# Kernel tuning notes

Hardware: AMD Instinct MI355X
Metric: run time of the kernel (lower is better)

Reference implementation:

```python
import jax, jax.numpy as jnp
import numpy as np

RESERVOIR_SIZE = 1024
D_MODEL = 512
BATCH = 256
SEQ_LEN = 512
SPECTRAL_RADIUS = 0.9
SPARSITY = 0.9
INPUT_SCALING = 1.0


def _build_reservoir_weights(seed=0):
    rng = np.random.default_rng(seed)
    W_in = rng.standard_normal((RESERVOIR_SIZE, 1)).astype(np.float32) * INPUT_SCALING
    W_res = rng.standard_normal((RESERVOIR_SIZE, RESERVOIR_SIZE)).astype(np.float32)
    # sparsify: zero out `sparsity` fraction of entries
    num_zeros = int(RESERVOIR_SIZE * RESERVOIR_SIZE * SPARSITY)
    flat = W_res.reshape(-1)
    zero_idx = rng.permutation(RESERVOIR_SIZE * RESERVOIR_SIZE)[:num_zeros]
    flat[zero_idx] = 0.0
    # rescale to target spectral radius
    eigs = np.linalg.eigvals(W_res.astype(np.float64))
    sr = np.max(np.abs(eigs))
    if sr > 1e-9:
        W_res *= np.float32(SPECTRAL_RADIUS / sr)
    return jnp.asarray(W_in), jnp.asarray(W_res)


def setup_inputs() -> dict:
    key = jax.random.key(0)
    kx, kw, kb = jax.random.split(key, 3)
    x = jax.random.normal(kx, (BATCH, SEQ_LEN), dtype=jnp.float32)
    W_in, W_res = _build_reservoir_weights(0)
    # trainable readout: Linear(reservoir_size, d_model)
    bound = 1.0 / np.sqrt(RESERVOIR_SIZE)
    readout_w = jax.random.uniform(kw, (D_MODEL, RESERVOIR_SIZE), jnp.float32, -bound, bound)
    readout_b = jax.random.uniform(kb, (D_MODEL,), jnp.float32, -bound, bound)
    return {"x": x, "W_in": W_in, "W_res": W_res,
            "readout_w": readout_w, "readout_b": readout_b}


def reference(x, W_in, W_res, readout_w, readout_b):
    # x: [B, S]; recurrence h_{t} = tanh(h_{t-1} @ W_res.T + u_t @ W_in.T)
    B = x.shape[0]
    h0 = jnp.zeros((B, RESERVOIR_SIZE), dtype=x.dtype)
    w_in_row = W_in[:, 0]  # [R]; u_t @ W_in.T == outer(u_t, w_in_row)

    def step(h, u_t):
        # u_t: [B]
        h_new = jnp.tanh(h @ W_res.T + u_t[:, None] * w_in_row[None, :])
        return h_new, None

    h_final, _ = jax.lax.scan(step, h0, x.T)  # scan over seq dim
    return h_final @ readout_w.T + readout_b  # [B, d_model]
```

## Files before the change

kernel.cpp:

```cpp
#include <hip/hip_runtime.h>

#define RES 1024
#define SEQ 512

typedef _Float16 f16;
typedef _Float16 half8 __attribute__((ext_vector_type(8)));
typedef float f32x4 __attribute__((ext_vector_type(4)));
typedef float f32x2 __attribute__((ext_vector_type(2), aligned(4)));
typedef unsigned int uint4v __attribute__((ext_vector_type(4)));

#define PST 35
#define PIDX(w8, n, rr, cc) ((((w8) * 4 + (n)) * 16 + (rr)) * PST + (cc))


__device__ __forceinline__ float fast_tanh(float v) {
  float vc = fminf(15.0f, fmaxf(-15.0f, v));
  float e = __expf(2.0f * vc);
  return (e - 1.0f) * __builtin_amdgcn_rcpf(e + 1.0f);
}

#define FULL_LOAD(ptr)                                                  \
  asm volatile(                                                         \
      "global_load_dwordx4 %0, %4, off sc0 sc1\n\t"                     \
      "global_load_dwordx4 %1, %4, off offset:64 sc0 sc1\n\t"           \
      "global_load_dwordx4 %2, %4, off offset:128 sc0 sc1\n\t"          \
      "global_load_dwordx4 %3, %4, off offset:192 sc0 sc1\n\t"          \
      "s_waitcnt vmcnt(0)"                                              \
      : "=&v"(A0), "=&v"(A1), "=&v"(A2), "=&v"(A3) : "v"(ptr) : "memory")

__device__ __forceinline__ bool tags_ok(half8 A0, half8 A1, half8 A2, half8 A3,
                                        unsigned int tagr) {
  const uint4v b0 = __builtin_bit_cast(uint4v, A0);
  const uint4v b1 = __builtin_bit_cast(uint4v, A1);
  const uint4v b2 = __builtin_bit_cast(uint4v, A2);
  const uint4v b3 = __builtin_bit_cast(uint4v, A3);
  unsigned int d =
      (b0.x ^ tagr) | (b0.y ^ tagr) | (b0.z ^ tagr) | (b0.w ^ tagr) |
      (b1.x ^ tagr) | (b1.y ^ tagr) | (b1.z ^ tagr) | (b1.w ^ tagr) |
      (b2.x ^ tagr) | (b2.y ^ tagr) | (b2.z ^ tagr) | (b2.w ^ tagr) |
      (b3.x ^ tagr) | (b3.y ^ tagr) | (b3.z ^ tagr) | (b3.w ^ tagr);
  return ((d & 1u) == 0u);
}

__global__ __launch_bounds__(512, 2) void res_recur_kernel(
    const float* __restrict__ x,
    const float* __restrict__ W_in,
    const float* __restrict__ W_res,
    f16* __restrict__ hp0,
    f16* __restrict__ hp1,
    f16* __restrict__ hm0,
    f16* __restrict__ hm1,
    unsigned int* __restrict__ xcdmap)
{
  __shared__ float P[20608];
  __shared__ unsigned char xmap_s[256];
  __shared__ int l2mode_s;

  const int tid  = threadIdx.x;
  const int wave = tid >> 6;
  const int lane = tid & 63;
  const int col  = lane & 15;
  const int kq   = (lane >> 4) & 3;

  const int bx = blockIdx.x;
  const int g  = (bx & 7) * 2 + ((bx >> 3) & 1);
  const int w  = bx >> 4;

  unsigned int myxcc;
  asm volatile("s_getreg_b32 %0, hwreg(HW_REG_XCC_ID, 0, 8)" : "=s"(myxcc));
  if (tid == 0)
    __hip_atomic_store(&xcdmap[bx], (myxcc & 0xffu) + 1u, __ATOMIC_RELAXED,
                       __HIP_MEMORY_SCOPE_AGENT);

  half8 Wf[4][4];
#pragma unroll
  for (int n = 0; n < 4; ++n) {
    const float* Wr = W_res + (size_t)(w * 64 + n * 16 + col) * RES + wave * 128 + kq * 8;
#pragma unroll
    for (int ks = 0; ks < 4; ++ks) {
      f32x4 lo = *(const f32x4*)(Wr + ks * 32);
      f32x4 hi = *(const f32x4*)(Wr + ks * 32 + 4);
      half8 f;
#pragma unroll
      for (int j = 0; j < 4; ++j) { f[j] = (f16)lo[j]; f[j + 4] = (f16)hi[j]; }
      Wf[n][ks] = f;
    }
  }

  if (tid < 256) {
    const unsigned int* ap = xcdmap + tid;
    unsigned int v;
    do {
      asm volatile("global_load_dword %0, %1, off sc0 sc1\n\t"
                   "s_waitcnt vmcnt(0)"
                   : "=&v"(v) : "v"(ap) : "memory");
    } while (v == 0u);
    xmap_s[tid] = (unsigned char)v;
  }
  __syncthreads();
  if (tid == 0) {
    const int base = (g >> 1) + 8 * (g & 1);
    const unsigned char ref = xmap_s[base];
    int ok = 1, cnt = 0;
    for (int i = 0; i < 256; ++i) cnt += (xmap_s[i] == ref) ? 1 : 0;
    for (int k = 0; k < 16; ++k) ok &= (xmap_s[base + 16 * k] == ref) ? 1 : 0;
    l2mode_s = (ok && cnt <= 64) ? 1 : 0;
  }
  __syncthreads();
  const bool l2mode = (l2mode_s != 0);

  const int r   = tid >> 5;
  const int cp  = tid & 31;
  const int n_e = cp >> 3;
  const int c0  = (cp & 7) * 2;
  const int rd_off = 12 - 4 * (r >> 2);
  const float win_lo = W_in[w * 64 + n_e * 16 + c0];
  const float win_hi = W_in[w * 64 + n_e * 16 + c0 + 1];
  const float* xr = x + (size_t)(g * 16 + r) * SEQ;
  const unsigned int houtidx = ((unsigned)(g * 16 + r) * RES + w * 64 + n_e * 16 + c0) >> 1;

  const size_t aoff = (size_t)(g * 16 + col) * RES + wave * 128 + kq * 8;

  for (int s = 0; s < SEQ; ++s) {
    float u = xr[s];

    f32x4 acc[4];
#pragma unroll
    for (int n = 0; n < 4; ++n) acc[n] = (f32x4){0.f, 0.f, 0.f, 0.f};

    if (s > 0) {
      const unsigned int tagr = (unsigned)(((s >> 1) + (s & 1)) & 1);
      const f16* Ap = ((s & 1) ? hp1 : hp0) + aoff;
      const f16* Am = ((s & 1) ? hm1 : hm0) + aoff;
      half8 A0, A1, A2, A3;

      FULL_LOAD(Ap);
      bool ok = tags_ok(A0, A1, A2, A3, tagr);
      unsigned int it = 0;
      while (!ok) {
        ++it;
        asm volatile("s_sleep 2");
        const f16* Pp = (!l2mode && ((it & 7u) == 0u)) ? Am : Ap;
        FULL_LOAD(Pp);
        ok = tags_ok(A0, A1, A2, A3, tagr);
      }

#pragma unroll
      for (int n = 0; n < 4; ++n) acc[n] = __builtin_amdgcn_mfma_f32_16x16x32_f16(A0, Wf[n][0], acc[n], 0, 0, 0);
#pragma unroll
      for (int n = 0; n < 4; ++n) acc[n] = __builtin_amdgcn_mfma_f32_16x16x32_f16(A1, Wf[n][1], acc[n], 0, 0, 0);
#pragma unroll
      for (int n = 0; n < 4; ++n) acc[n] = __builtin_amdgcn_mfma_f32_16x16x32_f16(A2, Wf[n][2], acc[n], 0, 0, 0);
#pragma unroll
      for (int n = 0; n < 4; ++n) acc[n] = __builtin_amdgcn_mfma_f32_16x16x32_f16(A3, Wf[n][3], acc[n], 0, 0, 0);
    }

#pragma unroll
    for (int n = 0; n < 4; ++n)
#pragma unroll
      for (int j = 0; j < 4; ++j)
        P[PIDX(wave, n, kq * 4 + j, col) + 12 - 4 * kq] = acc[n][j];

    __syncthreads();

    float s_lo = 0.f, s_hi = 0.f;
#pragma unroll
    for (int w8 = 0; w8 < 8; ++w8) {
      f32x2 t = *(const f32x2*)&P[PIDX(w8, n_e, r, c0) + rd_off];
      s_lo += t.x;
      s_hi += t.y;
    }
    float v_lo = fast_tanh(s_lo + u * win_lo);
    float v_hi = fast_tanh(s_hi + u * win_hi);

    const unsigned int tagw = (unsigned)((((s + 1) >> 1) + ((s + 1) & 1)) & 1);
    union { f16 h[2]; unsigned int u32; } pk;
    pk.h[0] = (f16)v_lo;
    pk.h[1] = (f16)v_hi;
    pk.u32  = (pk.u32 & ~1u) | tagw;

    unsigned int* Hp = (unsigned int*)((s & 1) ? hp0 : hp1);
    Hp[houtidx] = pk.u32;
    if (!l2mode) {
      unsigned int* Hm = (unsigned int*)((s & 1) ? hm0 : hm1);
      __hip_atomic_store(&Hm[houtidx], pk.u32, __ATOMIC_RELAXED,
                         __HIP_MEMORY_SCOPE_AGENT);
    }

    asm volatile("" ::: "memory");
    __builtin_amdgcn_s_barrier();
  }
}

__global__ __launch_bounds__(256) void res_readout_kernel(
    const f16* __restrict__ Hf,
    const float* __restrict__ Wout,
    const float* __restrict__ bout,
    float* __restrict__ out)
{
  __shared__ f16 hs[16][1032];
  __shared__ f16 wsh[32][1032];
  const int tid = threadIdx.x;
  const int bb = blockIdx.x >> 4;
  const int db = blockIdx.x & 15;

  for (int idx = tid; idx < 2048; idx += 256) {
    int row = idx >> 7, cin = idx & 127;
    *(half8*)&hs[row][cin * 8] = *(const half8*)(Hf + (size_t)(bb * 16 + row) * RES + cin * 8);
  }
  for (int idx = tid; idx < 4096; idx += 256) {
    int row = idx >> 7, cin = idx & 127;
    const float* p = Wout + (size_t)(db * 32 + row) * RES + cin * 8;
    f32x4 lo = *(const f32x4*)(p);
    f32x4 hi = *(const f32x4*)(p + 4);
    half8 f;
#pragma unroll
    for (int j = 0; j < 4; ++j) { f[j] = (f16)lo[j]; f[j + 4] = (f16)hi[j]; }
    *(half8*)&wsh[row][cin * 8] = f;
  }
  __syncthreads();

  const int d  = tid & 31;
  const int bp = tid >> 5;
  float acc0 = 0.f, acc1 = 0.f;
  for (int kc = 0; kc < 128; ++kc) {
    half8 wv = *(const half8*)&wsh[d][kc * 8];
    half8 h0 = *(const half8*)&hs[bp * 2][kc * 8];
    half8 h1 = *(const half8*)&hs[bp * 2 + 1][kc * 8];
#pragma unroll
    for (int j = 0; j < 8; ++j) {
      float wf = (float)wv[j];
      acc0 += wf * (float)h0[j];
      acc1 += wf * (float)h1[j];
    }
  }
  float bo = bout[db * 32 + d];
  out[(size_t)(bb * 16 + bp * 2) * 512 + db * 32 + d]     = acc0 + bo;
  out[(size_t)(bb * 16 + bp * 2 + 1) * 512 + db * 32 + d] = acc1 + bo;
}

extern "C" void kernel_launch(void* const* d_in, const int* in_sizes, int n_in,
                              void* d_out, int out_size, void* d_ws, size_t ws_size,
                              hipStream_t stream) {
  (void)in_sizes; (void)n_in; (void)out_size; (void)ws_size;
  const float* x     = (const float*)d_in[0];
  const float* W_in  = (const float*)d_in[1];
  const float* W_res = (const float*)d_in[2];
  const float* Wout  = (const float*)d_in[3];
  const float* bout  = (const float*)d_in[4];
  float* out = (float*)d_out;

  char* ws = (char*)d_ws;
  f16* hp0 = (f16*)(ws);
  f16* hp1 = (f16*)(ws + (512u << 10));
  f16* hm0 = (f16*)(ws + (1024u << 10));
  f16* hm1 = (f16*)(ws + (1536u << 10));
  unsigned int* xcdmap = (unsigned int*)(ws + (2048u << 10));

  hipMemsetAsync(ws, 0, (2048u << 10), stream);
  hipMemsetAsync(ws + (2048u << 10), 0, 1024, stream);

  res_recur_kernel<<<dim3(256), dim3(512), 0, stream>>>(x, W_in, W_res,
                                                        hp0, hp1, hm0, hm1, xcdmap);
  res_readout_kernel<<<dim3(256), dim3(256), 0, stream>>>(hp0, Wout, bout, out);
}
```

Baseline: 866.1 us.

## Split each recurrence step into two 8-row phases and stage x in LDS

```diff
diff --git a/kernel.cpp b/kernel.cpp
--- a/kernel.cpp
+++ b/kernel.cpp
@@ -52,7 +52,8 @@
     f16* __restrict__ hm1,
     unsigned int* __restrict__ xcdmap)
 {
-  __shared__ float P[20608];
+  __shared__ float P[17920];
+  __shared__ float x_s[16][512];
   __shared__ unsigned char xmap_s[256];
   __shared__ int l2mode_s;
 
@@ -63,7 +64,7 @@
   const int kq   = (lane >> 4) & 3;
 
   const int bx = blockIdx.x;
-  const int g  = (bx & 7) * 2 + ((bx >> 3) & 1);
+  const int p  = (bx & 7) * 2 + ((bx >> 3) & 1);
   const int w  = bx >> 4;
 
   unsigned int myxcc;
@@ -85,6 +86,11 @@
       for (int j = 0; j < 4; ++j) { f[j] = (f16)lo[j]; f[j + 4] = (f16)hi[j]; }
       Wf[n][ks] = f;
     }
+  }
+
+  for (int idx = tid; idx < 2048; idx += 512) {
+    int row = idx >> 7, c4 = (idx & 127) * 4;
+    *(f32x4*)&x_s[row][c4] = *(const f32x4*)(x + (size_t)(p * 16 + row) * SEQ + c4);
   }
 
   if (tid < 256) {
@@ -99,7 +105,7 @@
   }
   __syncthreads();
   if (tid == 0) {
-    const int base = (g >> 1) + 8 * (g & 1);
+    const int base = (p >> 1) + 8 * (p & 1);
     const unsigned char ref = xmap_s[base];
     int ok = 1, cnt = 0;
     for (int i = 0; i < 256; ++i) cnt += (xmap_s[i] == ref) ? 1 : 0;
@@ -110,85 +116,91 @@
   const bool l2mode = (l2mode_s != 0);
 
   const int r   = tid >> 5;
+  const int rr  = r & 7;
+  const bool active = (r < 8);
   const int cp  = tid & 31;
   const int n_e = cp >> 3;
   const int c0  = (cp & 7) * 2;
   const int rd_off = 12 - 4 * (r >> 2);
   const float win_lo = W_in[w * 64 + n_e * 16 + c0];
   const float win_hi = W_in[w * 64 + n_e * 16 + c0 + 1];
-  const float* xr = x + (size_t)(g * 16 + r) * SEQ;
-  const unsigned int houtidx = ((unsigned)(g * 16 + r) * RES + w * 64 + n_e * 16 + c0) >> 1;
-
-  const size_t aoff = (size_t)(g * 16 + col) * RES + wave * 128 + kq * 8;
+
+  const size_t aoff0 = (size_t)(p * 16 + (col & 7)) * RES + wave * 128 + kq * 8;
 
   for (int s = 0; s < SEQ; ++s) {
-    float u = xr[s];
-
-    f32x4 acc[4];
-#pragma unroll
-    for (int n = 0; n < 4; ++n) acc[n] = (f32x4){0.f, 0.f, 0.f, 0.f};
-
-    if (s > 0) {
-      const unsigned int tagr = (unsigned)(((s >> 1) + (s & 1)) & 1);
-      const f16* Ap = ((s & 1) ? hp1 : hp0) + aoff;
-      const f16* Am = ((s & 1) ? hm1 : hm0) + aoff;
-      half8 A0, A1, A2, A3;
-
-      FULL_LOAD(Ap);
-      bool ok = tags_ok(A0, A1, A2, A3, tagr);
-      unsigned int it = 0;
-      while (!ok) {
-        ++it;
-        asm volatile("s_sleep 2");
-        const f16* Pp = (!l2mode && ((it & 7u) == 0u)) ? Am : Ap;
-        FULL_LOAD(Pp);
-        ok = tags_ok(A0, A1, A2, A3, tagr);
+    const unsigned int tagr = (unsigned)(((s >> 1) + (s & 1)) & 1);
+    const unsigned int tagw = (unsigned)((((s + 1) >> 1) + ((s + 1) & 1)) & 1);
+
+    for (int ph = 0; ph < 2; ++ph) {
+      const int rb = ph << 3;
+      float u = x_s[rb + rr][s];
+
+      f32x4 acc[4];
+#pragma unroll
+      for (int n = 0; n < 4; ++n) acc[n] = (f32x4){0.f, 0.f, 0.f, 0.f};
+
+      if (s > 0) {
+        const f16* Ap = ((s & 1) ? hp1 : hp0) + aoff0 + (size_t)rb * RES;
+        const f16* Am = ((s & 1) ? hm1 : hm0) + aoff0 + (size_t)rb * RES;
+        half8 A0, A1, A2, A3;
+
+        FULL_LOAD(Ap);
+        bool ok = tags_ok(A0, A1, A2, A3, tagr);
+        unsigned int it = 0;
+        while (!ok) {
+          ++it;
+          const f16* Pp = (!l2mode && ((it & 7u) == 0u)) ? Am : Ap;
+          FULL_LOAD(Pp);
+          ok = tags_ok(A0, A1, A2, A3, tagr);
+        }
+
+#pragma unroll
+        for (int n = 0; n < 4; ++n) acc[n] = __builtin_amdgcn_mfma_f32_16x16x32_f16(A0, Wf[n][0], acc[n], 0, 0, 0);
+#pragma unroll
+        for (int n = 0; n < 4; ++n) acc[n] = __builtin_amdgcn_mfma_f32_16x16x32_f16(A1, Wf[n][1], acc[n], 0, 0, 0);
+#pragma unroll
+        for (int n = 0; n < 4; ++n) acc[n] = __builtin_amdgcn_mfma_f32_16x16x32_f16(A2, Wf[n][2], acc[n], 0, 0, 0);
+#pragma unroll
+        for (int n = 0; n < 4; ++n) acc[n] = __builtin_amdgcn_mfma_f32_16x16x32_f16(A3, Wf[n][3], acc[n], 0, 0, 0);
       }
 
 #pragma unroll
-      for (int n = 0; n < 4; ++n) acc[n] = __builtin_amdgcn_mfma_f32_16x16x32_f16(A0, Wf[n][0], acc[n], 0, 0, 0);
-#pragma unroll
-      for (int n = 0; n < 4; ++n) acc[n] = __builtin_amdgcn_mfma_f32_16x16x32_f16(A1, Wf[n][1], acc[n], 0, 0, 0);
-#pragma unroll
-      for (int n = 0; n < 4; ++n) acc[n] = __builtin_amdgcn_mfma_f32_16x16x32_f16(A2, Wf[n][2], acc[n], 0, 0, 0);
-#pragma unroll
-      for (int n = 0; n < 4; ++n) acc[n] = __builtin_amdgcn_mfma_f32_16x16x32_f16(A3, Wf[n][3], acc[n], 0, 0, 0);
+      for (int n = 0; n < 4; ++n)
+#pragma unroll
+        for (int j = 0; j < 4; ++j)
+          P[PIDX(wave, n, kq * 4 + j, col) + 12 - 4 * kq] = acc[n][j];
+
+      __syncthreads();
+
+      float s_lo = 0.f, s_hi = 0.f;
+#pragma unroll
+      for (int w8 = 0; w8 < 8; ++w8) {
+        f32x2 t = *(const f32x2*)&P[PIDX(w8, n_e, r, c0) + rd_off];
+        s_lo += t.x;
+        s_hi += t.y;
+      }
+      float v_lo = fast_tanh(s_lo + u * win_lo);
+      float v_hi = fast_tanh(s_hi + u * win_hi);
+
+      union { f16 h[2]; unsigned int u32; } pk;
+      pk.h[0] = (f16)v_lo;
+      pk.h[1] = (f16)v_hi;
+      pk.u32  = (pk.u32 & ~1u) | tagw;
+
+      if (active) {
+        const unsigned int houtidx =
+            ((unsigned)(p * 16 + rb + rr) * RES + w * 64 + n_e * 16 + c0) >> 1;
+        unsigned int* Hp = (unsigned int*)((s & 1) ? hp0 : hp1);
+        Hp[houtidx] = pk.u32;
+        if (!l2mode) {
+          unsigned int* Hm = (unsigned int*)((s & 1) ? hm0 : hm1);
+          __hip_atomic_store(&Hm[houtidx], pk.u32, __ATOMIC_RELAXED,
+                             __HIP_MEMORY_SCOPE_AGENT);
+        }
+      }
+
+      __syncthreads();
     }
-
-#pragma unroll
-    for (int n = 0; n < 4; ++n)
-#pragma unroll
-      for (int j = 0; j < 4; ++j)
-        P[PIDX(wave, n, kq * 4 + j, col) + 12 - 4 * kq] = acc[n][j];
-
-    __syncthreads();
-
-    float s_lo = 0.f, s_hi = 0.f;
-#pragma unroll
-    for (int w8 = 0; w8 < 8; ++w8) {
-      f32x2 t = *(const f32x2*)&P[PIDX(w8, n_e, r, c0) + rd_off];
-      s_lo += t.x;
-      s_hi += t.y;
-    }
-    float v_lo = fast_tanh(s_lo + u * win_lo);
-    float v_hi = fast_tanh(s_hi + u * win_hi);
-
-    const unsigned int tagw = (unsigned)((((s + 1) >> 1) + ((s + 1) & 1)) & 1);
-    union { f16 h[2]; unsigned int u32; } pk;
-    pk.h[0] = (f16)v_lo;
-    pk.h[1] = (f16)v_hi;
-    pk.u32  = (pk.u32 & ~1u) | tagw;
-
-    unsigned int* Hp = (unsigned int*)((s & 1) ? hp0 : hp1);
-    Hp[houtidx] = pk.u32;
-    if (!l2mode) {
-      unsigned int* Hm = (unsigned int*)((s & 1) ? hm0 : hm1);
-      __hip_atomic_store(&Hm[houtidx], pk.u32, __ATOMIC_RELAXED,
-                         __HIP_MEMORY_SCOPE_AGENT);
-    }
-
-    asm volatile("" ::: "memory");
-    __builtin_amdgcn_s_barrier();
   }
 }
 
```

Result: slower. 1.560 ms (+80.1%).

## Halve recurrence block to 4 waves with double-buffered LDS partials

Applied to the files above, without the earlier changes.

```diff
diff --git a/kernel.cpp b/kernel.cpp
--- a/kernel.cpp
+++ b/kernel.cpp
@@ -10,7 +10,8 @@
 typedef unsigned int uint4v __attribute__((ext_vector_type(4)));
 
 #define PST 35
-#define PIDX(w8, n, rr, cc) ((((w8) * 4 + (n)) * 16 + (rr)) * PST + (cc))
+#define PPL 10752
+#define PIDX(w4, n, rr, cc) ((((w4) * 4 + (n)) * 16 + (rr)) * PST + (cc))
 
 
 __device__ __forceinline__ float fast_tanh(float v) {
@@ -19,30 +20,32 @@
   return (e - 1.0f) * __builtin_amdgcn_rcpf(e + 1.0f);
 }
 
-#define FULL_LOAD(ptr)                                                  \
+#define FULL_LOAD8(ptr)                                                 \
   asm volatile(                                                         \
-      "global_load_dwordx4 %0, %4, off sc0 sc1\n\t"                     \
-      "global_load_dwordx4 %1, %4, off offset:64 sc0 sc1\n\t"           \
-      "global_load_dwordx4 %2, %4, off offset:128 sc0 sc1\n\t"          \
-      "global_load_dwordx4 %3, %4, off offset:192 sc0 sc1\n\t"          \
+      "global_load_dwordx4 %0, %8, off sc0 sc1\n\t"                     \
+      "global_load_dwordx4 %1, %8, off offset:64 sc0 sc1\n\t"           \
+      "global_load_dwordx4 %2, %8, off offset:128 sc0 sc1\n\t"          \
+      "global_load_dwordx4 %3, %8, off offset:192 sc0 sc1\n\t"          \
+      "global_load_dwordx4 %4, %8, off offset:256 sc0 sc1\n\t"          \
+      "global_load_dwordx4 %5, %8, off offset:320 sc0 sc1\n\t"          \
+      "global_load_dwordx4 %6, %8, off offset:384 sc0 sc1\n\t"          \
+      "global_load_dwordx4 %7, %8, off offset:448 sc0 sc1\n\t"          \
       "s_waitcnt vmcnt(0)"                                              \
-      : "=&v"(A0), "=&v"(A1), "=&v"(A2), "=&v"(A3) : "v"(ptr) : "memory")
-
-__device__ __forceinline__ bool tags_ok(half8 A0, half8 A1, half8 A2, half8 A3,
-                                        unsigned int tagr) {
-  const uint4v b0 = __builtin_bit_cast(uint4v, A0);
-  const uint4v b1 = __builtin_bit_cast(uint4v, A1);
-  const uint4v b2 = __builtin_bit_cast(uint4v, A2);
-  const uint4v b3 = __builtin_bit_cast(uint4v, A3);
-  unsigned int d =
-      (b0.x ^ tagr) | (b0.y ^ tagr) | (b0.z ^ tagr) | (b0.w ^ tagr) |
-      (b1.x ^ tagr) | (b1.y ^ tagr) | (b1.z ^ tagr) | (b1.w ^ tagr) |
-      (b2.x ^ tagr) | (b2.y ^ tagr) | (b2.z ^ tagr) | (b2.w ^ tagr) |
-      (b3.x ^ tagr) | (b3.y ^ tagr) | (b3.z ^ tagr) | (b3.w ^ tagr);
+      : "=&v"(A[0]), "=&v"(A[1]), "=&v"(A[2]), "=&v"(A[3]),             \
+        "=&v"(A[4]), "=&v"(A[5]), "=&v"(A[6]), "=&v"(A[7])              \
+      : "v"(ptr) : "memory")
+
+__device__ __forceinline__ bool tags_ok8(const half8* A, unsigned int tagr) {
+  unsigned int d = 0;
+#pragma unroll
+  for (int i = 0; i < 8; ++i) {
+    const uint4v b = __builtin_bit_cast(uint4v, A[i]);
+    d |= (b.x ^ tagr) | (b.y ^ tagr) | (b.z ^ tagr) | (b.w ^ tagr);
+  }
   return ((d & 1u) == 0u);
 }
 
-__global__ __launch_bounds__(512, 2) void res_recur_kernel(
+__global__ __launch_bounds__(256, 1) void res_recur_kernel(
     const float* __restrict__ x,
     const float* __restrict__ W_in,
     const float* __restrict__ W_res,
@@ -52,7 +55,7 @@
     f16* __restrict__ hm1,
     unsigned int* __restrict__ xcdmap)
 {
-  __shared__ float P[20608];
+  __shared__ float P[2][PPL];
   __shared__ unsigned char xmap_s[256];
   __shared__ int l2mode_s;
 
@@ -72,12 +75,12 @@
     __hip_atomic_store(&xcdmap[bx], (myxcc & 0xffu) + 1u, __ATOMIC_RELAXED,
                        __HIP_MEMORY_SCOPE_AGENT);
 
-  half8 Wf[4][4];
+  half8 Wf[4][8];
 #pragma unroll
   for (int n = 0; n < 4; ++n) {
-    const float* Wr = W_res + (size_t)(w * 64 + n * 16 + col) * RES + wave * 128 + kq * 8;
-#pragma unroll
-    for (int ks = 0; ks < 4; ++ks) {
+    const float* Wr = W_res + (size_t)(w * 64 + n * 16 + col) * RES + wave * 256 + kq * 8;
+#pragma unroll
+    for (int ks = 0; ks < 8; ++ks) {
       f32x4 lo = *(const f32x4*)(Wr + ks * 32);
       f32x4 hi = *(const f32x4*)(Wr + ks * 32 + 4);
       half8 f;
@@ -109,20 +112,23 @@
   __syncthreads();
   const bool l2mode = (l2mode_s != 0);
 
-  const int r   = tid >> 5;
-  const int cp  = tid & 31;
-  const int n_e = cp >> 3;
-  const int c0  = (cp & 7) * 2;
+  const int r   = tid >> 4;
+  const int te  = tid & 15;
+  const int n_e = te >> 2;
+  const int c0  = (te & 3) * 4;
   const int rd_off = 12 - 4 * (r >> 2);
-  const float win_lo = W_in[w * 64 + n_e * 16 + c0];
-  const float win_hi = W_in[w * 64 + n_e * 16 + c0 + 1];
+  const float win0 = W_in[w * 64 + n_e * 16 + c0];
+  const float win1 = W_in[w * 64 + n_e * 16 + c0 + 1];
+  const float win2 = W_in[w * 64 + n_e * 16 + c0 + 2];
+  const float win3 = W_in[w * 64 + n_e * 16 + c0 + 3];
   const float* xr = x + (size_t)(g * 16 + r) * SEQ;
   const unsigned int houtidx = ((unsigned)(g * 16 + r) * RES + w * 64 + n_e * 16 + c0) >> 1;
 
-  const size_t aoff = (size_t)(g * 16 + col) * RES + wave * 128 + kq * 8;
+  const size_t aoff = (size_t)(g * 16 + col) * RES + wave * 256 + kq * 8;
 
   for (int s = 0; s < SEQ; ++s) {
     float u = xr[s];
+    float* __restrict__ Pp = &P[s & 1][0];
 
     f32x4 acc[4];
 #pragma unroll
@@ -132,63 +138,62 @@
       const unsigned int tagr = (unsigned)(((s >> 1) + (s & 1)) & 1);
       const f16* Ap = ((s & 1) ? hp1 : hp0) + aoff;
       const f16* Am = ((s & 1) ? hm1 : hm0) + aoff;
-      half8 A0, A1, A2, A3;
-
-      FULL_LOAD(Ap);
-      bool ok = tags_ok(A0, A1, A2, A3, tagr);
+      half8 A[8];
+
+      FULL_LOAD8(Ap);
+      bool ok = tags_ok8(A, tagr);
       unsigned int it = 0;
       while (!ok) {
         ++it;
-        asm volatile("s_sleep 2");
-        const f16* Pp = (!l2mode && ((it & 7u) == 0u)) ? Am : Ap;
-        FULL_LOAD(Pp);
-        ok = tags_ok(A0, A1, A2, A3, tagr);
+        const f16* Pq = (!l2mode && ((it & 7u) == 0u)) ? Am : Ap;
+        FULL_LOAD8(Pq);
+        ok = tags_ok8(A, tagr);
       }
 
 #pragma unroll
-      for (int n = 0; n < 4; ++n) acc[n] = __builtin_amdgcn_mfma_f32_16x16x32_f16(A0, Wf[n][0], acc[n], 0, 0, 0);
-#pragma unroll
-      for (int n = 0; n < 4; ++n) acc[n] = __builtin_amdgcn_mfma_f32_16x16x32_f16(A1, Wf[n][1], acc[n], 0, 0, 0);
-#pragma unroll
-      for (int n = 0; n < 4; ++n) acc[n] = __builtin_amdgcn_mfma_f32_16x16x32_f16(A2, Wf[n][2], acc[n], 0, 0, 0);
-#pragma unroll
-      for (int n = 0; n < 4; ++n) acc[n] = __builtin_amdgcn_mfma_f32_16x16x32_f16(A3, Wf[n][3], acc[n], 0, 0, 0);
+      for (int ks = 0; ks < 8; ++ks)
+#pragma unroll
+        for (int n = 0; n < 4; ++n)
+          acc[n] = __builtin_amdgcn_mfma_f32_16x16x32_f16(A[ks], Wf[n][ks], acc[n], 0, 0, 0);
     }
 
 #pragma unroll
     for (int n = 0; n < 4; ++n)
 #pragma unroll
       for (int j = 0; j < 4; ++j)
-        P[PIDX(wave, n, kq * 4 + j, col) + 12 - 4 * kq] = acc[n][j];
+        Pp[PIDX(wave, n, kq * 4 + j, col) + 12 - 4 * kq] = acc[n][j];
 
     __syncthreads();
 
-    float s_lo = 0.f, s_hi = 0.f;
-#pragma unroll
-    for (int w8 = 0; w8 < 8; ++w8) {
-      f32x2 t = *(const f32x2*)&P[PIDX(w8, n_e, r, c0) + rd_off];
-      s_lo += t.x;
-      s_hi += t.y;
-    }
-    float v_lo = fast_tanh(s_lo + u * win_lo);
-    float v_hi = fast_tanh(s_hi + u * win_hi);
+    float s0 = 0.f, s1 = 0.f, s2 = 0.f, s3 = 0.f;
+#pragma unroll
+    for (int w4 = 0; w4 < 4; ++w4) {
+      f32x2 a = *(const f32x2*)&Pp[PIDX(w4, n_e, r, c0) + rd_off];
+      f32x2 b = *(const f32x2*)&Pp[PIDX(w4, n_e, r, c0 + 2) + rd_off];
+      s0 += a.x; s1 += a.y; s2 += b.x; s3 += b.y;
+    }
+    float v0 = fast_tanh(s0 + u * win0);
+    float v1 = fast_tanh(s1 + u * win1);
+    float v2 = fast_tanh(s2 + u * win2);
+    float v3 = fast_tanh(s3 + u * win3);
 
     const unsigned int tagw = (unsigned)((((s + 1) >> 1) + ((s + 1) & 1)) & 1);
-    union { f16 h[2]; unsigned int u32; } pk;
-    pk.h[0] = (f16)v_lo;
-    pk.h[1] = (f16)v_hi;
-    pk.u32  = (pk.u32 & ~1u) | tagw;
+    union { f16 h[2]; unsigned int u32; } pk0, pk1;
+    pk0.h[0] = (f16)v0; pk0.h[1] = (f16)v1;
+    pk1.h[0] = (f16)v2; pk1.h[1] = (f16)v3;
+    pk0.u32 = (pk0.u32 & ~1u) | tagw;
+    pk1.u32 = (pk1.u32 & ~1u) | tagw;
 
     unsigned int* Hp = (unsigned int*)((s & 1) ? hp0 : hp1);
-    Hp[houtidx] = pk.u32;
+    uint2 pv; pv.x = pk0.u32; pv.y = pk1.u32;
+    *(uint2*)&Hp[houtidx] = pv;
     if (!l2mode) {
       unsigned int* Hm = (unsigned int*)((s & 1) ? hm0 : hm1);
-      __hip_atomic_store(&Hm[houtidx], pk.u32, __ATOMIC_RELAXED,
+      __hip_atomic_store(&Hm[houtidx], pk0.u32, __ATOMIC_RELAXED,
                          __HIP_MEMORY_SCOPE_AGENT);
-    }
-
-    asm volatile("" ::: "memory");
-    __builtin_amdgcn_s_barrier();
+      __hip_atomic_store(&Hm[houtidx + 1], pk1.u32, __ATOMIC_RELAXED,
+                         __HIP_MEMORY_SCOPE_AGENT);
+    }
   }
 }
 
@@ -260,7 +265,7 @@
   hipMemsetAsync(ws, 0, (2048u << 10), stream);
   hipMemsetAsync(ws + (2048u << 10), 0, 1024, stream);
 
-  res_recur_kernel<<<dim3(256), dim3(512), 0, stream>>>(x, W_in, W_res,
+  res_recur_kernel<<<dim3(256), dim3(256), 0, stream>>>(x, W_in, W_res,
                                                         hp0, hp1, hm0, hm1, xcdmap);
   res_readout_kernel<<<dim3(256), dim3(256), 0, stream>>>(hp0, Wout, bout, out);
 }
```

Measured after the change: 1.102 ms. +27.2%, slower.
